# Performance work log

Hardware: AMD Instinct MI355X
Metric: run time of the kernel (lower is better)

## Reference

```python
import jax, jax.numpy as jnp
import numpy as np

B, L, D = 16, 2048, 128
GROUP = 16
NG = L // GROUP  # number of groups per batch
ALPHA = 0.5


def setup_inputs() -> dict:
    key = jax.random.key(0)
    k0, k1, k2 = jax.random.split(key, 3)
    x = jax.random.normal(k0, (B, L, D), dtype=jnp.float32)
    # per-batch permutation = gather indices (each position used exactly once)
    group_tensor = jax.vmap(lambda k: jax.random.permutation(k, L))(
        jax.random.split(k1, B)).astype(jnp.int32)
    ctxlens = jnp.full((B,), L, dtype=jnp.int32)
    W = jax.random.normal(k2, (2 * D,), dtype=jnp.float32) * (1.0 / np.sqrt(D))
    norm_alpha = jnp.ones((2,), dtype=jnp.float32)
    norm_gamma = jnp.ones((2 * D,), dtype=jnp.float32)
    norm_beta = jnp.zeros((2 * D,), dtype=jnp.float32)
    return {"x": x, "group_tensor": group_tensor, "ctxlens": ctxlens, "W": W,
            "norm_alpha": norm_alpha, "norm_gamma": norm_gamma, "norm_beta": norm_beta}


def _leaky_relu(v):
    return jnp.where(v >= 0, v, 0.01 * v)


def _ncn_forward(x, group_tensor, ctxlens, W, norm_alpha, norm_gamma, norm_beta):
    Bd, Ld, Dd = x.shape
    ng = Ld // GROUP
    Wi, Wj = W[:Dd], W[Dd:]
    a1, a2 = norm_alpha[0], norm_alpha[1]
    g1, g2 = norm_gamma[:Dd], norm_gamma[Dd:]
    b1, b2 = norm_beta[:Dd], norm_beta[Dd:]

    # gather x by group indices -> [B, NG, GROUP, D]
    xg = jnp.take_along_axis(x, group_tensor[:, :, None].astype(jnp.int32), axis=1)
    xg = xg.reshape(Bd, ng, GROUP, Dd)

    def step(carry, j):
        xi, xa = carry  # each [B, NG, GROUP, D]
        xj = jax.lax.dynamic_slice_in_dim(xi, j, 1, axis=2)  # [B, NG, 1, D]
        sim = jnp.einsum('bgnd,d->bgn', xi, Wi) \
            + jnp.einsum('bgd,d->bg', xj[:, :, 0, :], Wj)[:, :, None]  # [B,NG,GROUP]
        T = ALPHA * xi + (1.0 - ALPHA) * sim[..., None] * xj
        T_norm = g1 * jnp.tanh(a1 * T) + b1
        Fv = _leaky_relu(T_norm)
        xa = xa + Fv                               # ya = xa + F
        xi = xi + g2 * jnp.tanh(a2 * xa) + b2      # yi = xi + norm2(ya)
        return (xi, xa), None

    (yi, ya), _ = jax.lax.scan(step, (xg, jnp.zeros_like(xg)), jnp.arange(GROUP))

    # kernel only processes/stores a group if its start offset < ctxlen
    valid = (jnp.arange(ng, dtype=jnp.int32) * GROUP)[None, :] < ctxlens[:, None]
    yi = jnp.where(valid[:, :, None, None], yi, 0.0).reshape(Bd, Ld, Dd)
    ya = jnp.where(valid[:, :, None, None], ya, 0.0).reshape(Bd, Ld, Dd)

    # scatter back to original positions
    bidx = jnp.arange(Bd)[:, None]
    yi_out = jnp.zeros_like(x).at[bidx, group_tensor].set(yi)
    ya_out = jnp.zeros_like(x).at[bidx, group_tensor].set(ya)
    return yi_out, ya_out


def reference(x, group_tensor, ctxlens, W, norm_alpha, norm_gamma, norm_beta):
    return _ncn_forward(x, group_tensor, ctxlens, W, norm_alpha, norm_gamma, norm_beta)
```

## Files before the change

### kernel.cpp

```cpp
#include <hip/hip_runtime.h>

#define B_ 16
#define L_ 2048
#define D_ 128
#define GROUP_ 16
#define NG_ (L_ / GROUP_)
#define LOG2E_ 1.44269504088896340736f

typedef float v2 __attribute__((ext_vector_type(2)));

template<int CTRL>
__device__ __forceinline__ float dpp_add(float v) {
    int x = __builtin_amdgcn_update_dpp(0, __float_as_int(v), CTRL, 0xF, 0xF, false);
    return v + __int_as_float(x);
}

__device__ __forceinline__ float row32_sum(float v) {
    v = dpp_add<0xB1>(v);
    v = dpp_add<0x4E>(v);
    v = dpp_add<0x141>(v);
    v = dpp_add<0x140>(v);
    int s = __builtin_amdgcn_ds_swizzle(__float_as_int(v), 0x401F);
    return v + __int_as_float(s);
}

__global__ __launch_bounds__(512, 8) void ncn_kernel(
    const float* __restrict__ x,
    const int*   __restrict__ gt,
    const int*   __restrict__ ctxlens,
    const float* __restrict__ W,
    const float* __restrict__ nalpha,
    const float* __restrict__ ngamma,
    const float* __restrict__ nbeta,
    float* __restrict__ out)
{
    const int blk = blockIdx.x;
    const int b   = blk >> 7;
    const int g   = blk & (NG_ - 1);
    const int tid = threadIdx.x;
    const int row = tid >> 5;
    const int rl  = tid & 31;
    const int d0  = rl << 2;

    __shared__ float s_xj[2][D_];

    const float a1 = nalpha[0];
    const float a2 = nalpha[1];
    const float ca = -a1 * LOG2E_;
    const float S  = -2.0f * a2 * LOG2E_;
    const bool  selMin = (S < 0.0f);

    v2 Wi[2], Wj[2], G1S[2], B1S[2], G2[2], B2[2];
    {
        float4 w  = *(const float4*)(W + d0);
        float4 wv = *(const float4*)(W + D_ + d0);
        Wi[0] = (v2){w.x,  w.y};  Wi[1] = (v2){w.z,  w.w};
        Wj[0] = (v2){wv.x, wv.y}; Wj[1] = (v2){wv.z, wv.w};

        float4 g1 = *(const float4*)(ngamma + d0);
        float4 g2 = *(const float4*)(ngamma + D_ + d0);
        float4 b1 = *(const float4*)(nbeta + d0);
        float4 b2 = *(const float4*)(nbeta + D_ + d0);
        v2 g1v[2] = {(v2){g1.x, g1.y}, (v2){g1.z, g1.w}};
        v2 g2v[2] = {(v2){g2.x, g2.y}, (v2){g2.z, g2.w}};
        v2 b1v[2] = {(v2){b1.x, b1.y}, (v2){b1.z, b1.w}};
        v2 b2v[2] = {(v2){b2.x, b2.y}, (v2){b2.z, b2.w}};
#pragma unroll
        for (int k = 0; k < 2; ++k) {
            G1S[k] = (S * 2.0f) * g1v[k];
            B1S[k] = S * (b1v[k] - g1v[k]);
            G2[k]  = 2.0f * g2v[k];
            B2[k]  = b2v[k] - g2v[k];
        }
    }

    const int l   = g * GROUP_ + row;
    const int tok = gt[b * L_ + l];
    const float* xp = x + ((size_t)(b * L_ + tok)) * D_ + d0;

    v2 xi[2], za[2];
    float4 xA = *(const float4*)xp;
    xi[0] = (v2){xA.x, xA.y}; xi[1] = (v2){xA.z, xA.w};
    za[0] = (v2){0.0f, 0.0f}; za[1] = (v2){0.0f, 0.0f};

    if (row == 0) *(float4*)&s_xj[0][d0] = xA;
    __syncthreads();

#pragma unroll 2
    for (int j = 0; j < GROUP_; ++j) {
        const int p = j & 1;

        v2 xjv[2];
        {
            float4 t = *(const float4*)&s_xj[p][d0];
            xjv[0] = (v2){t.x, t.y}; xjv[1] = (v2){t.z, t.w};
        }

        v2 sv = (v2){0.0f, 0.0f};
        sv = __builtin_elementwise_fma(xi[0],  Wi[0], sv);
        sv = __builtin_elementwise_fma(xi[1],  Wi[1], sv);
        sv = __builtin_elementwise_fma(xjv[0], Wj[0], sv);
        sv = __builtin_elementwise_fma(xjv[1], Wj[1], sv);
        const float sim = row32_sum(sv.x + sv.y);

        const v2 simv = (v2){sim, sim};
        const v2 cav  = (v2){ca, ca};
        const v2 onev = (v2){1.0f, 1.0f};
        const v2 leak = (v2){0.01f, 0.01f};

#pragma unroll
        for (int k = 0; k < 2; ++k) {
            v2 T2 = __builtin_elementwise_fma(simv, xjv[k], xi[k]);
            v2 u  = cav * T2;
            v2 e1 = (v2){__builtin_amdgcn_exp2f(u.x), __builtin_amdgcn_exp2f(u.y)};
            v2 d1 = e1 + onev;
            v2 r1 = (v2){__builtin_amdgcn_rcpf(d1.x), __builtin_amdgcn_rcpf(d1.y)};
            v2 tnS = __builtin_elementwise_fma(G1S[k], r1, B1S[k]);
            v2 alt = tnS * leak;
            v2 FvS = selMin ? __builtin_elementwise_min(tnS, alt)
                            : __builtin_elementwise_max(tnS, alt);
            za[k] += FvS;
            v2 e2 = (v2){__builtin_amdgcn_exp2f(za[k].x), __builtin_amdgcn_exp2f(za[k].y)};
            v2 d2 = e2 + onev;
            v2 r2 = (v2){__builtin_amdgcn_rcpf(d2.x), __builtin_amdgcn_rcpf(d2.y)};
            xi[k] = __builtin_elementwise_fma(G2[k], r2, xi[k] + B2[k]);
        }

        if (j + 1 < GROUP_ && row == j + 1) {
            float4 o = {xi[0].x, xi[0].y, xi[1].x, xi[1].y};
            *(float4*)&s_xj[p ^ 1][d0] = o;
        }
        __syncthreads();
    }

    const float invS = 1.0f / S;
    const v2 invSv = (v2){invS, invS};
    v2 xa[2];
    xa[0] = za[0] * invSv;
    xa[1] = za[1] * invSv;

    const bool valid = (g * GROUP_) < ctxlens[b];
    if (!valid) {
        xi[0] = (v2){0, 0}; xi[1] = (v2){0, 0};
        xa[0] = (v2){0, 0}; xa[1] = (v2){0, 0};
    }

    float* o1 = out + ((size_t)(b * L_ + tok)) * D_ + d0;
    float* o2 = o1 + (size_t)B_ * L_ * D_;
    float4 s1 = {xi[0].x, xi[0].y, xi[1].x, xi[1].y};
    float4 s2 = {xa[0].x, xa[0].y, xa[1].x, xa[1].y};
    *(float4*)o1 = s1;
    *(float4*)o2 = s2;
}

extern "C" void kernel_launch(void* const* d_in, const int* in_sizes, int n_in,
                              void* d_out, int out_size, void* d_ws, size_t ws_size,
                              hipStream_t stream) {
    const float* x  = (const float*)d_in[0];
    const int*   gt = (const int*)d_in[1];
    const int*   cl = (const int*)d_in[2];
    const float* W  = (const float*)d_in[3];
    const float* na = (const float*)d_in[4];
    const float* ng = (const float*)d_in[5];
    const float* nb = (const float*)d_in[6];
    float* out = (float*)d_out;

    ncn_kernel<<<B_ * NG_, 512, 0, stream>>>(x, gt, cl, W, na, ng, nb, out);
}
```

Baseline: 117.7 us.

## Process each group in a single wavefront with all rows held in registers

Restructures the kernel so that one 64-lane wavefront handles an entire 16-token group, with each lane owning two feature dims for all 16 rows in registers. This removes the shared-memory broadcast of xj and the per-step block-wide __syncthreads. The per-row dot products become 16 interleaved wave reductions using DPP, swizzle and bpermute. In exchange, blocks are smaller (2048 single-wave blocks), register pressure is much higher, and global loads and stores are only 8 bytes per lane.

```diff
diff --git a/kernel.cpp b/kernel.cpp
--- a/kernel.cpp
+++ b/kernel.cpp
@@ -10,21 +10,12 @@
 typedef float v2 __attribute__((ext_vector_type(2)));
 
 template<int CTRL>
-__device__ __forceinline__ float dpp_add(float v) {
-    int x = __builtin_amdgcn_update_dpp(0, __float_as_int(v), CTRL, 0xF, 0xF, false);
-    return v + __int_as_float(x);
+__device__ __forceinline__ float dpp_mov(float v) {
+    return __int_as_float(
+        __builtin_amdgcn_update_dpp(0, __float_as_int(v), CTRL, 0xF, 0xF, false));
 }
 
-__device__ __forceinline__ float row32_sum(float v) {
-    v = dpp_add<0xB1>(v);
-    v = dpp_add<0x4E>(v);
-    v = dpp_add<0x141>(v);
-    v = dpp_add<0x140>(v);
-    int s = __builtin_amdgcn_ds_swizzle(__float_as_int(v), 0x401F);
-    return v + __int_as_float(s);
-}
-
-__global__ __launch_bounds__(512, 8) void ncn_kernel(
+__global__ __launch_bounds__(64, 2) void ncn_kernel(
     const float* __restrict__ x,
     const int*   __restrict__ gt,
     const int*   __restrict__ ctxlens,
@@ -34,15 +25,11 @@
     const float* __restrict__ nbeta,
     float* __restrict__ out)
 {
-    const int blk = blockIdx.x;
-    const int b   = blk >> 7;
-    const int g   = blk & (NG_ - 1);
-    const int tid = threadIdx.x;
-    const int row = tid >> 5;
-    const int rl  = tid & 31;
-    const int d0  = rl << 2;
-
-    __shared__ float s_xj[2][D_];
+    const int blk  = blockIdx.x;
+    const int b    = blk >> 7;
+    const int g    = blk & (NG_ - 1);
+    const int lane = threadIdx.x;
+    const int d0   = lane << 1;
 
     const float a1 = nalpha[0];
     const float a2 = nalpha[1];
@@ -50,107 +37,117 @@
     const float S  = -2.0f * a2 * LOG2E_;
     const bool  selMin = (S < 0.0f);
 
-    v2 Wi[2], Wj[2], G1S[2], B1S[2], G2[2], B2[2];
+    v2 Wiv, Wjv, G1S, B1S, G2v, B2v;
     {
-        float4 w  = *(const float4*)(W + d0);
-        float4 wv = *(const float4*)(W + D_ + d0);
-        Wi[0] = (v2){w.x,  w.y};  Wi[1] = (v2){w.z,  w.w};
-        Wj[0] = (v2){wv.x, wv.y}; Wj[1] = (v2){wv.z, wv.w};
-
-        float4 g1 = *(const float4*)(ngamma + d0);
-        float4 g2 = *(const float4*)(ngamma + D_ + d0);
-        float4 b1 = *(const float4*)(nbeta + d0);
-        float4 b2 = *(const float4*)(nbeta + D_ + d0);
-        v2 g1v[2] = {(v2){g1.x, g1.y}, (v2){g1.z, g1.w}};
-        v2 g2v[2] = {(v2){g2.x, g2.y}, (v2){g2.z, g2.w}};
-        v2 b1v[2] = {(v2){b1.x, b1.y}, (v2){b1.z, b1.w}};
-        v2 b2v[2] = {(v2){b2.x, b2.y}, (v2){b2.z, b2.w}};
-#pragma unroll
-        for (int k = 0; k < 2; ++k) {
-            G1S[k] = (S * 2.0f) * g1v[k];
-            B1S[k] = S * (b1v[k] - g1v[k]);
-            G2[k]  = 2.0f * g2v[k];
-            B2[k]  = b2v[k] - g2v[k];
-        }
+        Wiv = *(const v2*)(W + d0);
+        Wjv = *(const v2*)(W + D_ + d0);
+        v2 g1 = *(const v2*)(ngamma + d0);
+        v2 g2 = *(const v2*)(ngamma + D_ + d0);
+        v2 b1 = *(const v2*)(nbeta + d0);
+        v2 b2 = *(const v2*)(nbeta + D_ + d0);
+        G1S = (S * 2.0f) * g1;
+        B1S = S * (b1 - g1);
+        G2v = 2.0f * g2;
+        B2v = b2 - g2;
     }
 
-    const int l   = g * GROUP_ + row;
-    const int tok = gt[b * L_ + l];
-    const float* xp = x + ((size_t)(b * L_ + tok)) * D_ + d0;
+    const int* gtp = gt + b * L_ + g * GROUP_;
+    int tok[GROUP_];
+#pragma unroll
+    for (int r = 0; r < GROUP_; ++r) tok[r] = gtp[r];
 
-    v2 xi[2], za[2];
-    float4 xA = *(const float4*)xp;
-    xi[0] = (v2){xA.x, xA.y}; xi[1] = (v2){xA.z, xA.w};
-    za[0] = (v2){0.0f, 0.0f}; za[1] = (v2){0.0f, 0.0f};
+    v2 xi[GROUP_], za[GROUP_];
+#pragma unroll
+    for (int r = 0; r < GROUP_; ++r) {
+        xi[r] = *(const v2*)(x + ((size_t)(b * L_ + tok[r])) * D_ + d0);
+        za[r] = (v2){0.0f, 0.0f};
+    }
 
-    if (row == 0) *(float4*)&s_xj[0][d0] = xA;
-    __syncthreads();
+    v2 xj = xi[0];
+    const int xaddr = (lane ^ 32) << 2;
 
-#pragma unroll 2
+    const v2 cav  = (v2){ca, ca};
+    const v2 onev = (v2){1.0f, 1.0f};
+    const v2 leak = (v2){0.01f, 0.01f};
+
+#pragma unroll 1
     for (int j = 0; j < GROUP_; ++j) {
-        const int p = j & 1;
+        v2 pj = xj * Wjv;
+        v2 p[GROUP_];
+#pragma unroll
+        for (int r = 0; r < GROUP_; ++r)
+            p[r] = __builtin_elementwise_fma(xi[r], Wiv, pj);
 
-        v2 xjv[2];
-        {
-            float4 t = *(const float4*)&s_xj[p][d0];
-            xjv[0] = (v2){t.x, t.y}; xjv[1] = (v2){t.z, t.w};
+        v2 q[8];
+#pragma unroll
+        for (int k = 0; k < 8; ++k)
+            q[k] = (v2){p[2 * k].x + p[2 * k].y, p[2 * k + 1].x + p[2 * k + 1].y};
+
+#pragma unroll
+        for (int k = 0; k < 8; ++k) { v2 t = {dpp_mov<0xB1>(q[k].x),  dpp_mov<0xB1>(q[k].y)};  q[k] += t; }
+#pragma unroll
+        for (int k = 0; k < 8; ++k) { v2 t = {dpp_mov<0x4E>(q[k].x),  dpp_mov<0x4E>(q[k].y)};  q[k] += t; }
+#pragma unroll
+        for (int k = 0; k < 8; ++k) { v2 t = {dpp_mov<0x141>(q[k].x), dpp_mov<0x141>(q[k].y)}; q[k] += t; }
+#pragma unroll
+        for (int k = 0; k < 8; ++k) { v2 t = {dpp_mov<0x140>(q[k].x), dpp_mov<0x140>(q[k].y)}; q[k] += t; }
+#pragma unroll
+        for (int k = 0; k < 8; ++k) {
+            v2 t;
+            t.x = __int_as_float(__builtin_amdgcn_ds_swizzle(__float_as_int(q[k].x), 0x401F));
+            t.y = __int_as_float(__builtin_amdgcn_ds_swizzle(__float_as_int(q[k].y), 0x401F));
+            q[k] += t;
+        }
+#pragma unroll
+        for (int k = 0; k < 8; ++k) {
+            v2 t;
+            t.x = __int_as_float(__builtin_amdgcn_ds_bpermute(xaddr, __float_as_int(q[k].x)));
+            t.y = __int_as_float(__builtin_amdgcn_ds_bpermute(xaddr, __float_as_int(q[k].y)));
+            q[k] += t;
         }
 
-        v2 sv = (v2){0.0f, 0.0f};
-        sv = __builtin_elementwise_fma(xi[0],  Wi[0], sv);
-        sv = __builtin_elementwise_fma(xi[1],  Wi[1], sv);
-        sv = __builtin_elementwise_fma(xjv[0], Wj[0], sv);
-        sv = __builtin_elementwise_fma(xjv[1], Wj[1], sv);
-        const float sim = row32_sum(sv.x + sv.y);
-
-        const v2 simv = (v2){sim, sim};
-        const v2 cav  = (v2){ca, ca};
-        const v2 onev = (v2){1.0f, 1.0f};
-        const v2 leak = (v2){0.01f, 0.01f};
+        const int jn = j + 1;
+        v2 xj_next = xj;
 
 #pragma unroll
-        for (int k = 0; k < 2; ++k) {
-            v2 T2 = __builtin_elementwise_fma(simv, xjv[k], xi[k]);
+        for (int r = 0; r < GROUP_; ++r) {
+            const float s  = (r & 1) ? q[r >> 1].y : q[r >> 1].x;
+            const v2 simv  = (v2){s, s};
+            v2 T2 = __builtin_elementwise_fma(simv, xj, xi[r]);
             v2 u  = cav * T2;
             v2 e1 = (v2){__builtin_amdgcn_exp2f(u.x), __builtin_amdgcn_exp2f(u.y)};
             v2 d1 = e1 + onev;
             v2 r1 = (v2){__builtin_amdgcn_rcpf(d1.x), __builtin_amdgcn_rcpf(d1.y)};
-            v2 tnS = __builtin_elementwise_fma(G1S[k], r1, B1S[k]);
+            v2 tnS = __builtin_elementwise_fma(G1S, r1, B1S);
             v2 alt = tnS * leak;
             v2 FvS = selMin ? __builtin_elementwise_min(tnS, alt)
                             : __builtin_elementwise_max(tnS, alt);
-            za[k] += FvS;
-            v2 e2 = (v2){__builtin_amdgcn_exp2f(za[k].x), __builtin_amdgcn_exp2f(za[k].y)};
+            za[r] += FvS;
+            v2 e2 = (v2){__builtin_amdgcn_exp2f(za[r].x), __builtin_amdgcn_exp2f(za[r].y)};
             v2 d2 = e2 + onev;
             v2 r2 = (v2){__builtin_amdgcn_rcpf(d2.x), __builtin_amdgcn_rcpf(d2.y)};
-            xi[k] = __builtin_elementwise_fma(G2[k], r2, xi[k] + B2[k]);
+            xi[r] = __builtin_elementwise_fma(G2v, r2, xi[r] + B2v);
+            if (r == jn) xj_next = xi[r];
         }
-
-        if (j + 1 < GROUP_ && row == j + 1) {
-            float4 o = {xi[0].x, xi[0].y, xi[1].x, xi[1].y};
-            *(float4*)&s_xj[p ^ 1][d0] = o;
-        }
-        __syncthreads();
+        xj = xj_next;
     }
 
     const float invS = 1.0f / S;
     const v2 invSv = (v2){invS, invS};
-    v2 xa[2];
-    xa[0] = za[0] * invSv;
-    xa[1] = za[1] * invSv;
 
     const bool valid = (g * GROUP_) < ctxlens[b];
-    if (!valid) {
-        xi[0] = (v2){0, 0}; xi[1] = (v2){0, 0};
-        xa[0] = (v2){0, 0}; xa[1] = (v2){0, 0};
+
+    float* o1 = out + d0;
+    float* o2 = o1 + (size_t)B_ * L_ * D_;
+#pragma unroll
+    for (int r = 0; r < GROUP_; ++r) {
+        v2 yi = xi[r];
+        v2 ya = za[r] * invSv;
+        if (!valid) { yi = (v2){0, 0}; ya = (v2){0, 0}; }
+        const size_t off = ((size_t)(b * L_ + tok[r])) * D_;
+        *(v2*)(o1 + off) = yi;
+        *(v2*)(o2 + off) = ya;
     }
-
-    float* o1 = out + ((size_t)(b * L_ + tok)) * D_ + d0;
-    float* o2 = o1 + (size_t)B_ * L_ * D_;
-    float4 s1 = {xi[0].x, xi[0].y, xi[1].x, xi[1].y};
-    float4 s2 = {xa[0].x, xa[0].y, xa[1].x, xa[1].y};
-    *(float4*)o1 = s1;
-    *(float4*)o2 = s2;
 }
 
 extern "C" void kernel_launch(void* const* d_in, const int* in_sizes, int n_in,
@@ -165,5 +162,5 @@
     const float* nb = (const float*)d_in[6];
     float* out = (float*)d_out;
 
-    ncn_kernel<<<B_ * NG_, 512, 0, stream>>>(x, gt, cl, W, na, ng, nb, out);
+    ncn_kernel<<<B_ * NG_, 64, 0, stream>>>(x, gt, cl, W, na, ng, nb, out);
 }
```

After: 133.1 us. 1.13x slower.
